# Kernel tuning notes

Measured on AMD Instinct MI355X. Metric: run time of the kernel, lower is better.

The kernel has to match this reference:

```python
import jax, jax.numpy as jnp
import numpy as np

B, L, D, H, DH, FF = 4, 1024, 1024, 16, 64, 4096
EPS = 1e-5


def _layer_norm(x, g, b):
    m = jnp.mean(x, -1, keepdims=True)
    v = jnp.mean((x - m) ** 2, -1, keepdims=True)
    return (x - m) * jax.lax.rsqrt(v + EPS) * g + b


def setup_inputs() -> dict:
    key = jax.random.key(0)
    ks = jax.random.split(key, 20)
    s = 0.02  # param init scale
    return {
        "x": jax.random.normal(ks[0], (B, L, D), jnp.float32),
        "adj_mask_matrix": jax.random.uniform(ks[1], (B * H, L, L), jnp.float32),
        "com_mask_matrix": jax.random.uniform(ks[2], (B * H, L, L), jnp.float32),
        "lattice_rel": jax.random.normal(ks[3], (2, 1, 1, DH), jnp.float32),
        "Wq": jax.random.normal(ks[4], (D, D), jnp.float32) * s,
        "bq": jnp.zeros((D,), jnp.float32),
        "Wk": jax.random.normal(ks[5], (D, D), jnp.float32) * s,
        "bk": jnp.zeros((D,), jnp.float32),
        "Wv": jax.random.normal(ks[6], (D, D), jnp.float32) * s,
        "bv": jnp.zeros((D,), jnp.float32),
        "Wo": jax.random.normal(ks[7], (D, D), jnp.float32) * s,
        "bo": jnp.zeros((D,), jnp.float32),
        "ln1_scale": jnp.ones((D,), jnp.float32),
        "ln1_bias": jnp.zeros((D,), jnp.float32),
        "W1": jax.random.normal(ks[8], (D, FF), jnp.float32) * s,
        "b1": jnp.zeros((FF,), jnp.float32),
        "W2": jax.random.normal(ks[9], (FF, D), jnp.float32) * s,
        "b2": jnp.zeros((D,), jnp.float32),
        "ln2_scale": jnp.ones((D,), jnp.float32),
        "ln2_bias": jnp.zeros((D,), jnp.float32),
    }


def reference(x, adj_mask_matrix, com_mask_matrix, lattice_rel,
              Wq, bq, Wk, bk, Wv, bv, Wo, bo, ln1_scale, ln1_bias,
              W1, b1, W2, b2, ln2_scale, ln2_bias):
    Bsz, Ln, Dm = x.shape
    # QKV projections; flat reshape [B,L,H*dh] -> [B*H,L,dh] matches torch .view
    Q = (x @ Wq + bq).reshape(Bsz * H, Ln, DH)
    K = (x @ Wk + bk).reshape(Bsz * H, Ln, DH)
    V = (x @ Wv + bv).reshape(Bsz * H, Ln, DH)
    scale = DH ** (-0.5)
    adj_rel = lattice_rel[0]  # [1,1,dh] broadcasts over (B*H, L)
    com_rel = lattice_rel[1]
    att_adj = jnp.einsum('bqd,bkd->bqk', Q + adj_rel, K + adj_rel) * scale
    att_com = jnp.einsum('bqd,bkd->bqk', Q + com_rel, K + com_rel) * scale
    # post-softmax multiplicative masking, then sum of the two attention maps
    mask_att = (jax.nn.softmax(att_adj, axis=-1) * adj_mask_matrix
                + jax.nn.softmax(att_com, axis=-1) * com_mask_matrix)
    context = jnp.matmul(mask_att, V).reshape(Bsz, Ln, H * DH)
    out = _layer_norm(context @ Wo + bo + x, ln1_scale, ln1_bias)
    ff = jax.nn.relu(out @ W1 + b1) @ W2 + b2
    return _layer_norm(ff + out, ln2_scale, ln2_bias)
```

## Files before the change

### kernel.cpp

```cpp
#include <hip/hip_runtime.h>
#include <hip/hip_bf16.h>

typedef __attribute__((ext_vector_type(8))) short s16x8;
typedef __attribute__((ext_vector_type(4))) float f32x4;
typedef unsigned short u16;
typedef unsigned int u32;

__device__ __forceinline__ u16 f2b(float f) {
    u32 u = __float_as_uint(f);
    u32 r = (u + 0x7fffu + ((u >> 16) & 1u)) >> 16;
    return (u16)r;
}
__device__ __forceinline__ float b2f(u16 b) {
    return __uint_as_float(((u32)b) << 16);
}

#define MFMA16(a, b, c) __builtin_amdgcn_mfma_f32_16x16x32_bf16(a, b, c, 0, 0, 0)
#define GLDS(gp, lp)                                                              \
    __builtin_amdgcn_global_load_lds((const __attribute__((address_space(1))) void*)(gp), \
                                     (__attribute__((address_space(3))) void*)(lp), 16, 0, 0)

__global__ void k_f2b(const float* __restrict__ in, u16* __restrict__ out, int n4) {
    int i = blockIdx.x * 256 + threadIdx.x;
    if (i >= n4) return;
    float4 v = ((const float4*)in)[i];
    ushort4 o;
    o.x = f2b(v.x); o.y = f2b(v.y); o.z = f2b(v.z); o.w = f2b(v.w);
    ((ushort4*)out)[i] = o;
}

__global__ void k_wtrans(const float* __restrict__ W, u16* __restrict__ Wt, int K, int N) {
    __shared__ float t[32][33];
    int bx = blockIdx.x * 32, by = blockIdx.y * 32;
    int tx = threadIdx.x, ty = threadIdx.y;
    for (int i = 0; i < 32; i += 8)
        t[ty + i][tx] = W[(size_t)(by + ty + i) * N + bx + tx];
    __syncthreads();
    for (int i = 0; i < 32; i += 8)
        Wt[(size_t)(bx + ty + i) * K + by + tx] = f2b(t[tx][ty + i]);
}

__global__ __launch_bounds__(256) void gemm_qkv(const u16* __restrict__ A, const u16* __restrict__ Bt,
                                                const float* __restrict__ bq, const float* __restrict__ bk,
                                                const float* __restrict__ bv, const float* __restrict__ rel,
                                                u16* __restrict__ Qa, u16* __restrict__ Qc,
                                                u16* __restrict__ Ka, u16* __restrict__ Kc,
                                                u16* __restrict__ Vt) {
    __shared__ __align__(16) short lA[128 * 64];
    __shared__ __align__(16) short lB[128 * 64];
    const int tid = threadIdx.x, lane = tid & 63, w = tid >> 6;
    const int l15 = lane & 15, lg = lane >> 4;
    const int wr = w >> 1, wc = w & 1;
    const int m0 = blockIdx.y * 128, n0 = blockIdx.x * 128;
    const int KK = 1024;
    f32x4 acc[4][4] = {};

    for (int k0 = 0; k0 < KK; k0 += 64) {
        #pragma unroll
        for (int i = 0; i < 4; i++) {
            int chunk = w * 4 + i;
            int arow = m0 + chunk * 8 + (lane >> 3);
            GLDS(A + (size_t)arow * KK + k0 + (lane & 7) * 8, (short*)lA + chunk * 512);
            int brow = n0 + chunk * 8 + (lane >> 3);
            GLDS(Bt + (size_t)brow * KK + k0 + (lane & 7) * 8, (short*)lB + chunk * 512);
        }
        __syncthreads();
        #pragma unroll
        for (int ks = 0; ks < 2; ks++) {
            s16x8 af[4], bfr[4];
            #pragma unroll
            for (int m = 0; m < 4; m++)
                af[m] = *(const s16x8*)&lA[(wr * 64 + m * 16 + l15) * 64 + ks * 32 + lg * 8];
            #pragma unroll
            for (int n = 0; n < 4; n++)
                bfr[n] = *(const s16x8*)&lB[(wc * 64 + n * 16 + l15) * 64 + ks * 32 + lg * 8];
            #pragma unroll
            for (int m = 0; m < 4; m++)
                #pragma unroll
                for (int n = 0; n < 4; n++)
                    acc[m][n] = MFMA16(af[m], bfr[n], acc[m][n]);
        }
        __syncthreads();
    }
    const int rbase = m0 + wr * 64, cbase = n0 + wc * 64;
    const int seg = cbase >> 10;
    #pragma unroll
    for (int m = 0; m < 4; m++)
        #pragma unroll
        for (int n = 0; n < 4; n++) {
            int col = cbase + n * 16 + l15;
            int c1 = col & 1023, d = col & 63;
            int row0 = rbase + m * 16 + lg * 4;
            if (seg == 0) {
                float bb = bq[c1], r0 = rel[d], r1 = rel[64 + d];
                #pragma unroll
                for (int r = 0; r < 4; r++) {
                    float v = acc[m][n][r] + bb;
                    size_t o = (size_t)(row0 + r) * 1024 + c1;
                    Qa[o] = f2b(v + r0);
                    Qc[o] = f2b(v + r1);
                }
            } else if (seg == 1) {
                float bb = bk[c1], r0 = rel[d], r1 = rel[64 + d];
                #pragma unroll
                for (int r = 0; r < 4; r++) {
                    float v = acc[m][n][r] + bb;
                    size_t o = (size_t)(row0 + r) * 1024 + c1;
                    Ka[o] = f2b(v + r0);
                    Kc[o] = f2b(v + r1);
                }
            } else {
                float bb = bv[c1];
                #pragma unroll
                for (int r = 0; r < 4; r++) {
                    int row = row0 + r;
                    size_t o = (size_t)(row >> 6) * 65536 + (size_t)d * 1024 + (row & 63) * 16 + (c1 >> 6);
                    Vt[o] = f2b(acc[m][n][r] + bb);
                }
            }
        }
}

template <int EPI>
__global__ __launch_bounds__(256) void gemm_bt(const u16* __restrict__ A, const u16* __restrict__ Bt,
                                               void* __restrict__ Cv, int M, int N, int K,
                                               const float* __restrict__ bias) {
    __shared__ __align__(16) short lA[128 * 64];
    __shared__ __align__(16) short lB[128 * 64];
    const int tid = threadIdx.x, lane = tid & 63, w = tid >> 6;
    const int l15 = lane & 15, lg = lane >> 4;
    const int wr = w >> 1, wc = w & 1;
    const int m0 = blockIdx.y * 128, n0 = blockIdx.x * 128;
    f32x4 acc[4][4] = {};

    for (int k0 = 0; k0 < K; k0 += 64) {
        #pragma unroll
        for (int i = 0; i < 4; i++) {
            int chunk = w * 4 + i;
            int arow = m0 + chunk * 8 + (lane >> 3);
            GLDS(A + (size_t)arow * K + k0 + (lane & 7) * 8, (short*)lA + chunk * 512);
            int brow = n0 + chunk * 8 + (lane >> 3);
            GLDS(Bt + (size_t)brow * K + k0 + (lane & 7) * 8, (short*)lB + chunk * 512);
        }
        __syncthreads();
        #pragma unroll
        for (int ks = 0; ks < 2; ks++) {
            s16x8 af[4], bfr[4];
            #pragma unroll
            for (int m = 0; m < 4; m++)
                af[m] = *(const s16x8*)&lA[(wr * 64 + m * 16 + l15) * 64 + ks * 32 + lg * 8];
            #pragma unroll
            for (int n = 0; n < 4; n++)
                bfr[n] = *(const s16x8*)&lB[(wc * 64 + n * 16 + l15) * 64 + ks * 32 + lg * 8];
            #pragma unroll
            for (int m = 0; m < 4; m++)
                #pragma unroll
                for (int n = 0; n < 4; n++)
                    acc[m][n] = MFMA16(af[m], bfr[n], acc[m][n]);
        }
        __syncthreads();
    }
    const int rbase = m0 + wr * 64, cbase = n0 + wc * 64;
    #pragma unroll
    for (int m = 0; m < 4; m++)
        #pragma unroll
        for (int n = 0; n < 4; n++) {
            int col = cbase + n * 16 + l15;
            int row0 = rbase + m * 16 + lg * 4;
            u16* C = (u16*)Cv;
            float bv = bias[col];
            #pragma unroll
            for (int r = 0; r < 4; r++)
                C[(size_t)(row0 + r) * N + col] = f2b(fmaxf(acc[m][n][r] + bv, 0.f));
        }
}

__global__ __launch_bounds__(256) void gemm_bt64(const u16* __restrict__ A, const u16* __restrict__ Bt,
                                                 float* __restrict__ C, int M, int N, int K) {
    __shared__ __align__(16) short lA[128 * 64];
    __shared__ __align__(16) short lB[64 * 64];
    const int tid = threadIdx.x, lane = tid & 63, w = tid >> 6;
    const int l15 = lane & 15, lg = lane >> 4;
    const int m0 = blockIdx.y * 128, n0 = blockIdx.x * 64;
    f32x4 acc[2][4] = {};

    for (int k0 = 0; k0 < K; k0 += 64) {
        #pragma unroll
        for (int i = 0; i < 4; i++) {
            int chunk = w * 4 + i;
            int arow = m0 + chunk * 8 + (lane >> 3);
            GLDS(A + (size_t)arow * K + k0 + (lane & 7) * 8, (short*)lA + chunk * 512);
        }
        #pragma unroll
        for (int i = 0; i < 2; i++) {
            int chunk = w * 2 + i;
            int brow = n0 + chunk * 8 + (lane >> 3);
            GLDS(Bt + (size_t)brow * K + k0 + (lane & 7) * 8, (short*)lB + chunk * 512);
        }
        __syncthreads();
        #pragma unroll
        for (int ks = 0; ks < 2; ks++) {
            s16x8 af[2], bfr[4];
            #pragma unroll
            for (int m = 0; m < 2; m++)
                af[m] = *(const s16x8*)&lA[(w * 32 + m * 16 + l15) * 64 + ks * 32 + lg * 8];
            #pragma unroll
            for (int n = 0; n < 4; n++)
                bfr[n] = *(const s16x8*)&lB[(n * 16 + l15) * 64 + ks * 32 + lg * 8];
            #pragma unroll
            for (int m = 0; m < 2; m++)
                #pragma unroll
                for (int n = 0; n < 4; n++)
                    acc[m][n] = MFMA16(af[m], bfr[n], acc[m][n]);
        }
        __syncthreads();
    }
    #pragma unroll
    for (int m = 0; m < 2; m++)
        #pragma unroll
        for (int n = 0; n < 4; n++) {
            int col = n0 + n * 16 + l15;
            int row0 = m0 + w * 32 + m * 16 + lg * 4;
            #pragma unroll
            for (int r = 0; r < 4; r++)
                C[(size_t)(row0 + r) * N + col] = acc[m][n][r];
        }
}

__global__ __launch_bounds__(256, 2) void k_qke2(const u16* __restrict__ Qa, const u16* __restrict__ Qc,
                                                 const u16* __restrict__ Ka, const u16* __restrict__ Kc,
                                                 u16* __restrict__ Ea, u16* __restrict__ Ec,
                                                 float* __restrict__ denA, float* __restrict__ denC) {
    const int bid = blockIdx.x;
    const int xcd = bid & 7, j = bid >> 3;
    const int g = xcd * 8 + (j & 7), qt = j >> 3;
    const int tid = threadIdx.x, lane = tid & 63, w = tid >> 6;
    const int l15 = lane & 15, lg = lane >> 4;
    __shared__ __align__(16) float lE[2][4][16][68];

    const int q0 = qt * 64 + w * 16;
    const size_t gQ = (size_t)g * 65536;
    const size_t ebase = ((((size_t)g * 16 + qt) * 4 + w) * 16384) + (size_t)lane * 8;
    const float scale = 0.125f;

    s16x8 qa[2], qc[2];
    #pragma unroll
    for (int ks = 0; ks < 2; ks++) {
        size_t off = gQ + (size_t)(q0 + l15) * 64 + ks * 32 + lg * 8;
        qa[ks] = *(const s16x8*)(Qa + off);
        qc[ks] = *(const s16x8*)(Qc + off);
    }

    float la[4] = {0.f, 0.f, 0.f, 0.f}, lc[4] = {0.f, 0.f, 0.f, 0.f};

    #pragma unroll 1
    for (int it = 0; it < 16; it++) {
        const int kb = it * 64;
        f32x4 sa[4] = {}, sc[4] = {};
        s16x8 kfa[8], kfc[8];
        #pragma unroll
        for (int ks = 0; ks < 2; ks++)
            #pragma unroll
            for (int n = 0; n < 4; n++) {
                size_t koff = gQ + (size_t)(kb + n * 16 + l15) * 64 + ks * 32 + lg * 8;
                kfa[ks * 4 + n] = *(const s16x8*)(Ka + koff);
                kfc[ks * 4 + n] = *(const s16x8*)(Kc + koff);
            }
        #pragma unroll
        for (int ks = 0; ks < 2; ks++)
            #pragma unroll
            for (int n = 0; n < 4; n++) {
                sa[n] = MFMA16(qa[ks], kfa[ks * 4 + n], sa[n]);
                sc[n] = MFMA16(qc[ks], kfc[ks * 4 + n], sc[n]);
            }
        #pragma unroll
        for (int n = 0; n < 4; n++)
            #pragma unroll
            for (int r = 0; r < 4; r++) {
                float ea = __expf(sa[n][r] * scale);
                float ec = __expf(sc[n][r] * scale);
                la[r] += ea;
                lc[r] += ec;
                lE[0][w][lg * 4 + r][n * 16 + l15] = ea;
                lE[1][w][lg * 4 + r][n * 16 + l15] = ec;
            }
        #pragma unroll
        for (int ks = 0; ks < 2; ks++) {
            const float* ep = &lE[0][w][l15][ks * 32 + lg * 8];
            float4 e0 = *(const float4*)ep, e1 = *(const float4*)(ep + 4);
            uint4 st;
            st.x = (u32)f2b(e0.x) | ((u32)f2b(e0.y) << 16);
            st.y = (u32)f2b(e0.z) | ((u32)f2b(e0.w) << 16);
            st.z = (u32)f2b(e1.x) | ((u32)f2b(e1.y) << 16);
            st.w = (u32)f2b(e1.z) | ((u32)f2b(e1.w) << 16);
            *(uint4*)(Ea + ebase + (size_t)it * 1024 + ks * 512) = st;
            const float* fp = &lE[1][w][l15][ks * 32 + lg * 8];
            float4 f0 = *(const float4*)fp, f1 = *(const float4*)(fp + 4);
            uint4 st2;
            st2.x = (u32)f2b(f0.x) | ((u32)f2b(f0.y) << 16);
            st2.y = (u32)f2b(f0.z) | ((u32)f2b(f0.w) << 16);
            st2.z = (u32)f2b(f1.x) | ((u32)f2b(f1.y) << 16);
            st2.w = (u32)f2b(f1.z) | ((u32)f2b(f1.w) << 16);
            *(uint4*)(Ec + ebase + (size_t)it * 1024 + ks * 512) = st2;
        }
    }
    #pragma unroll
    for (int r = 0; r < 4; r++)
        #pragma unroll
        for (int m = 8; m >= 1; m >>= 1) {
            la[r] += __shfl_xor(la[r], m);
            lc[r] += __shfl_xor(lc[r], m);
        }
    if (l15 == 0) {
        #pragma unroll
        for (int r = 0; r < 4; r++) {
            denA[g * 1024 + q0 + lg * 4 + r] = la[r];
            denC[g * 1024 + q0 + lg * 4 + r] = lc[r];
        }
    }
}

__global__ __launch_bounds__(256, 2) void k_pv2(const u16* __restrict__ Ea, const u16* __restrict__ Ec,
                                                const u16* __restrict__ Vt,
                                                const float* __restrict__ adjm, const float* __restrict__ comm,
                                                const float* __restrict__ denA, const float* __restrict__ denC,
                                                u16* __restrict__ ctx) {
    const int bid = blockIdx.x;
    const int xcd = bid & 7, j = bid >> 3;
    const int g = xcd * 8 + (j & 7), qt = j >> 3;
    const int tid = threadIdx.x, lane = tid & 63, w = tid >> 6;
    const int l15 = lane & 15, lg = lane >> 4;

    const int q0 = qt * 64 + w * 16;
    const size_t gQ = (size_t)g * 65536;
    const size_t mroff = (size_t)g * 1048576 + (size_t)(q0 + l15) * 1024 + lg * 8;
    const float* __restrict__ mrow_a = adjm + mroff;
    const float* __restrict__ mrow_c = comm + mroff;
    const size_t ebase = ((((size_t)g * 16 + qt) * 4 + w) * 16384) + (size_t)lane * 8;

    f32x4 ca[4] = {}, cc[4] = {};

    #pragma unroll 2
    for (int it = 0; it < 16; it++) {
        const int kb = it * 64;
        s16x8 ea[2], ec[2], vf[8];
        float4 ma[4], mc[4];
        #pragma unroll
        for (int ks = 0; ks < 2; ks++) {
            ma[ks * 2 + 0] = *(const float4*)(mrow_a + kb + ks * 32);
            ma[ks * 2 + 1] = *(const float4*)(mrow_a + kb + ks * 32 + 4);
            mc[ks * 2 + 0] = *(const float4*)(mrow_c + kb + ks * 32);
            mc[ks * 2 + 1] = *(const float4*)(mrow_c + kb + ks * 32 + 4);
        }
        #pragma unroll
        for (int ks = 0; ks < 2; ks++) {
            ea[ks] = *(const s16x8*)(Ea + ebase + (size_t)it * 1024 + ks * 512);
            ec[ks] = *(const s16x8*)(Ec + ebase + (size_t)it * 1024 + ks * 512);
        }
        #pragma unroll
        for (int ks = 0; ks < 2; ks++)
            #pragma unroll
            for (int d = 0; d < 4; d++)
                vf[ks * 4 + d] = *(const s16x8*)(Vt + gQ + (size_t)(d * 16 + l15) * 1024 + kb + ks * 32 + lg * 8);
        #pragma unroll
        for (int ks = 0; ks < 2; ks++) {
            union { s16x8 v; u16 u[8]; } pa, pc;
            pa.u[0] = f2b(b2f((u16)ea[ks][0]) * ma[ks * 2].x);
            pa.u[1] = f2b(b2f((u16)ea[ks][1]) * ma[ks * 2].y);
            pa.u[2] = f2b(b2f((u16)ea[ks][2]) * ma[ks * 2].z);
            pa.u[3] = f2b(b2f((u16)ea[ks][3]) * ma[ks * 2].w);
            pa.u[4] = f2b(b2f((u16)ea[ks][4]) * ma[ks * 2 + 1].x);
            pa.u[5] = f2b(b2f((u16)ea[ks][5]) * ma[ks * 2 + 1].y);
            pa.u[6] = f2b(b2f((u16)ea[ks][6]) * ma[ks * 2 + 1].z);
            pa.u[7] = f2b(b2f((u16)ea[ks][7]) * ma[ks * 2 + 1].w);
            pc.u[0] = f2b(b2f((u16)ec[ks][0]) * mc[ks * 2].x);
            pc.u[1] = f2b(b2f((u16)ec[ks][1]) * mc[ks * 2].y);
            pc.u[2] = f2b(b2f((u16)ec[ks][2]) * mc[ks * 2].z);
            pc.u[3] = f2b(b2f((u16)ec[ks][3]) * mc[ks * 2].w);
            pc.u[4] = f2b(b2f((u16)ec[ks][4]) * mc[ks * 2 + 1].x);
            pc.u[5] = f2b(b2f((u16)ec[ks][5]) * mc[ks * 2 + 1].y);
            pc.u[6] = f2b(b2f((u16)ec[ks][6]) * mc[ks * 2 + 1].z);
            pc.u[7] = f2b(b2f((u16)ec[ks][7]) * mc[ks * 2 + 1].w);
            #pragma unroll
            for (int d = 0; d < 4; d++) {
                ca[d] = MFMA16(pa.v, vf[ks * 4 + d], ca[d]);
                cc[d] = MFMA16(pc.v, vf[ks * 4 + d], cc[d]);
            }
        }
    }
    float ila[4], ilc[4];
    #pragma unroll
    for (int r = 0; r < 4; r++) {
        ila[r] = 1.f / denA[g * 1024 + q0 + lg * 4 + r];
        ilc[r] = 1.f / denC[g * 1024 + q0 + lg * 4 + r];
    }
    #pragma unroll
    for (int r = 0; r < 4; r++) {
        int row = q0 + lg * 4 + r;
        #pragma unroll
        for (int d = 0; d < 4; d++)
            ctx[gQ + (size_t)row * 64 + d * 16 + l15] = f2b(ca[d][r] * ila[r] + cc[d][r] * ilc[r]);
    }
}

__global__ __launch_bounds__(256) void k_ln(const float* __restrict__ a, const float* __restrict__ bias,
                                            const float* __restrict__ resid, const float* __restrict__ gamma,
                                            const float* __restrict__ beta, float* __restrict__ out,
                                            u16* __restrict__ outb) {
    const int row = blockIdx.x, tid = threadIdx.x;
    const size_t base = (size_t)row * 1024 + tid * 4;
    float4 av = *(const float4*)(a + base);
    float4 rv = *(const float4*)(resid + base);
    float4 bv = *(const float4*)(bias + tid * 4);
    float t0 = av.x + rv.x + bv.x, t1 = av.y + rv.y + bv.y;
    float t2 = av.z + rv.z + bv.z, t3 = av.w + rv.w + bv.w;
    __shared__ float red[4];
    float s = t0 + t1 + t2 + t3;
    #pragma unroll
    for (int m = 32; m >= 1; m >>= 1) s += __shfl_xor(s, m);
    int w = tid >> 6;
    if ((tid & 63) == 0) red[w] = s;
    __syncthreads();
    float mean = (red[0] + red[1] + red[2] + red[3]) * (1.f / 1024.f);
    float d0 = t0 - mean, d1 = t1 - mean, d2 = t2 - mean, d3 = t3 - mean;
    float q = d0 * d0 + d1 * d1 + d2 * d2 + d3 * d3;
    __syncthreads();
    #pragma unroll
    for (int m = 32; m >= 1; m >>= 1) q += __shfl_xor(q, m);
    if ((tid & 63) == 0) red[w] = q;
    __syncthreads();
    float var = (red[0] + red[1] + red[2] + red[3]) * (1.f / 1024.f);
    float rs = rsqrtf(var + 1e-5f);
    float4 gv = *(const float4*)(gamma + tid * 4);
    float4 bev = *(const float4*)(beta + tid * 4);
    float o0 = d0 * rs * gv.x + bev.x, o1 = d1 * rs * gv.y + bev.y;
    float o2 = d2 * rs * gv.z + bev.z, o3 = d3 * rs * gv.w + bev.w;
    *(float4*)(out + base) = make_float4(o0, o1, o2, o3);
    if (outb) {
        ushort4 ob;
        ob.x = f2b(o0); ob.y = f2b(o1); ob.z = f2b(o2); ob.w = f2b(o3);
        *(ushort4*)(outb + base) = ob;
    }
}

extern "C" void kernel_launch(void* const* d_in, const int* in_sizes, int n_in,
                              void* d_out, int out_size, void* d_ws, size_t ws_size,
                              hipStream_t stream) {
    const float* x    = (const float*)d_in[0];
    const float* adjm = (const float*)d_in[1];
    const float* comm = (const float*)d_in[2];
    const float* rel  = (const float*)d_in[3];
    const float* Wq   = (const float*)d_in[4];
    const float* bq   = (const float*)d_in[5];
    const float* Wk   = (const float*)d_in[6];
    const float* bk   = (const float*)d_in[7];
    const float* Wv   = (const float*)d_in[8];
    const float* bv   = (const float*)d_in[9];
    const float* Wo   = (const float*)d_in[10];
    const float* bo   = (const float*)d_in[11];
    const float* g1   = (const float*)d_in[12];
    const float* be1  = (const float*)d_in[13];
    const float* W1   = (const float*)d_in[14];
    const float* b1   = (const float*)d_in[15];
    const float* W2   = (const float*)d_in[16];
    const float* b2   = (const float*)d_in[17];
    const float* g2   = (const float*)d_in[18];
    const float* be2  = (const float*)d_in[19];
    float* out = (float*)d_out;

    char* ws = (char*)d_ws;
    const size_t MB = 1048576;
    u16*   xb    = (u16*)(ws + 0 * MB);
    u16*   Wqkvt = (u16*)(ws + 8 * MB);
    u16*   Wot   = (u16*)(ws + 14 * MB);
    u16*   W1t   = (u16*)(ws + 16 * MB);
    u16*   W2t   = (u16*)(ws + 24 * MB);
    u16*   Qab   = (u16*)(ws + 32 * MB);
    u16*   Qcb   = (u16*)(ws + 40 * MB);
    u16*   Kab   = (u16*)(ws + 48 * MB);
    u16*   Kcb   = (u16*)(ws + 56 * MB);
    u16*   Vtb   = (u16*)(ws + 64 * MB);
    u16*   Eab   = (u16*)(ws + 72 * MB);
    u16*   Ecb   = (u16*)(ws + 200 * MB);
    float* denA  = (float*)(ws + 328 * MB);
    float* denC  = (float*)(ws + 329 * MB);
    u16*   ctx   = (u16*)(ws + 330 * MB);
    float* ctxWo = (float*)(ws + 32 * MB);
    float* out1  = (float*)(ws + 48 * MB);
    u16*   out1b = (u16*)(ws + 64 * MB);
    u16*   rb    = (u16*)(ws + 72 * MB);
    float* ff2   = (float*)(ws + 0 * MB);

    dim3 tb(32, 8);
    k_f2b<<<4096, 256, 0, stream>>>(x, xb, 1048576);
    k_wtrans<<<dim3(32, 32), tb, 0, stream>>>(Wq, Wqkvt, 1024, 1024);
    k_wtrans<<<dim3(32, 32), tb, 0, stream>>>(Wk, Wqkvt + 1024 * 1024, 1024, 1024);
    k_wtrans<<<dim3(32, 32), tb, 0, stream>>>(Wv, Wqkvt + 2 * 1024 * 1024, 1024, 1024);
    k_wtrans<<<dim3(32, 32), tb, 0, stream>>>(Wo, Wot, 1024, 1024);
    k_wtrans<<<dim3(128, 32), tb, 0, stream>>>(W1, W1t, 1024, 4096);
    k_wtrans<<<dim3(32, 128), tb, 0, stream>>>(W2, W2t, 4096, 1024);
    gemm_qkv<<<dim3(24, 32), 256, 0, stream>>>(xb, Wqkvt, bq, bk, bv, rel,
                                               Qab, Qcb, Kab, Kcb, Vtb);
    k_qke2<<<1024, 256, 0, stream>>>(Qab, Qcb, Kab, Kcb, Eab, Ecb, denA, denC);
    k_pv2<<<1024, 256, 0, stream>>>(Eab, Ecb, Vtb, adjm, comm, denA, denC, ctx);
    gemm_bt64<<<dim3(16, 32), 256, 0, stream>>>(ctx, Wot, ctxWo, 4096, 1024, 1024);
    k_ln<<<4096, 256, 0, stream>>>(ctxWo, bo, x, g1, be1, out1, out1b);
    gemm_bt<1><<<dim3(32, 32), 256, 0, stream>>>(out1b, W1t, rb, 4096, 4096, 1024, b1);
    gemm_bt64<<<dim3(16, 32), 256, 0, stream>>>(rb, W2t, ff2, 4096, 1024, 4096);
    k_ln<<<4096, 256, 0, stream>>>(ff2, b2, out1, g2, be2, out, nullptr);
}
```

Baseline: 654.1 us.

## Split attention key dimension in two halves with partial sums and combine kernel

The QK-exp and PV attention kernels now split the 1024 keys into two halves, doubling the grid from 1024 to 2048 blocks. Each half writes its own partial softmax denominators and an fp32 partial context. PV sums the two denominator halves before normalizing, and a new combine kernel adds the two partial contexts and converts them to bf16. This buys more parallelism per launch, but costs an extra fp32 write and read of the context, one more launch, and more denominator traffic.

```diff
diff --git a/kernel.cpp b/kernel.cpp
--- a/kernel.cpp
+++ b/kernel.cpp
@@ -230,10 +230,12 @@
 __global__ __launch_bounds__(256, 2) void k_qke2(const u16* __restrict__ Qa, const u16* __restrict__ Qc,
                                                  const u16* __restrict__ Ka, const u16* __restrict__ Kc,
                                                  u16* __restrict__ Ea, u16* __restrict__ Ec,
-                                                 float* __restrict__ denA, float* __restrict__ denC) {
+                                                 float* __restrict__ denA2, float* __restrict__ denC2) {
     const int bid = blockIdx.x;
     const int xcd = bid & 7, j = bid >> 3;
-    const int g = xcd * 8 + (j & 7), qt = j >> 3;
+    const int g = xcd * 8 + (j & 7);
+    const int rest = j >> 3;
+    const int qt = rest & 15, h = rest >> 4;
     const int tid = threadIdx.x, lane = tid & 63, w = tid >> 6;
     const int l15 = lane & 15, lg = lane >> 4;
     __shared__ __align__(16) float lE[2][4][16][68];
@@ -254,7 +256,7 @@
     float la[4] = {0.f, 0.f, 0.f, 0.f}, lc[4] = {0.f, 0.f, 0.f, 0.f};
 
     #pragma unroll 1
-    for (int it = 0; it < 16; it++) {
+    for (int it = h * 8; it < h * 8 + 8; it++) {
         const int kb = it * 64;
         f32x4 sa[4] = {}, sc[4] = {};
         s16x8 kfa[8], kfc[8];
@@ -314,8 +316,8 @@
     if (l15 == 0) {
         #pragma unroll
         for (int r = 0; r < 4; r++) {
-            denA[g * 1024 + q0 + lg * 4 + r] = la[r];
-            denC[g * 1024 + q0 + lg * 4 + r] = lc[r];
+            denA2[h * 65536 + g * 1024 + q0 + lg * 4 + r] = la[r];
+            denC2[h * 65536 + g * 1024 + q0 + lg * 4 + r] = lc[r];
         }
     }
 }
@@ -323,11 +325,13 @@
 __global__ __launch_bounds__(256, 2) void k_pv2(const u16* __restrict__ Ea, const u16* __restrict__ Ec,
                                                 const u16* __restrict__ Vt,
                                                 const float* __restrict__ adjm, const float* __restrict__ comm,
-                                                const float* __restrict__ denA, const float* __restrict__ denC,
-                                                u16* __restrict__ ctx) {
+                                                const float* __restrict__ denA2, const float* __restrict__ denC2,
+                                                float* __restrict__ ctxP) {
     const int bid = blockIdx.x;
     const int xcd = bid & 7, j = bid >> 3;
-    const int g = xcd * 8 + (j & 7), qt = j >> 3;
+    const int g = xcd * 8 + (j & 7);
+    const int rest = j >> 3;
+    const int qt = rest & 15, h = rest >> 4;
     const int tid = threadIdx.x, lane = tid & 63, w = tid >> 6;
     const int l15 = lane & 15, lg = lane >> 4;
 
@@ -341,7 +345,7 @@
     f32x4 ca[4] = {}, cc[4] = {};
 
     #pragma unroll 2
-    for (int it = 0; it < 16; it++) {
+    for (int it = h * 8; it < h * 8 + 8; it++) {
         const int kb = it * 64;
         s16x8 ea[2], ec[2], vf[8];
         float4 ma[4], mc[4];
@@ -391,16 +395,29 @@
     float ila[4], ilc[4];
     #pragma unroll
     for (int r = 0; r < 4; r++) {
-        ila[r] = 1.f / denA[g * 1024 + q0 + lg * 4 + r];
-        ilc[r] = 1.f / denC[g * 1024 + q0 + lg * 4 + r];
+        int idx = g * 1024 + q0 + lg * 4 + r;
+        ila[r] = 1.f / (denA2[idx] + denA2[65536 + idx]);
+        ilc[r] = 1.f / (denC2[idx] + denC2[65536 + idx]);
     }
     #pragma unroll
     for (int r = 0; r < 4; r++) {
         int row = q0 + lg * 4 + r;
         #pragma unroll
         for (int d = 0; d < 4; d++)
-            ctx[gQ + (size_t)row * 64 + d * 16 + l15] = f2b(ca[d][r] * ila[r] + cc[d][r] * ilc[r]);
-    }
+            ctxP[(size_t)h * 4194304 + gQ + (size_t)row * 64 + d * 16 + l15] =
+                ca[d][r] * ila[r] + cc[d][r] * ilc[r];
+    }
+}
+
+__global__ void k_comb2(const float* __restrict__ P, u16* __restrict__ out, int n4) {
+    int i = blockIdx.x * 256 + threadIdx.x;
+    if (i >= n4) return;
+    float4 a = ((const float4*)P)[i];
+    float4 c = ((const float4*)(P + 4194304))[i];
+    ushort4 o;
+    o.x = f2b(a.x + c.x); o.y = f2b(a.y + c.y);
+    o.z = f2b(a.z + c.z); o.w = f2b(a.w + c.w);
+    ((ushort4*)out)[i] = o;
 }
 
 __global__ __launch_bounds__(256) void k_ln(const float* __restrict__ a, const float* __restrict__ bias,
@@ -482,9 +499,10 @@
     u16*   Vtb   = (u16*)(ws + 64 * MB);
     u16*   Eab   = (u16*)(ws + 72 * MB);
     u16*   Ecb   = (u16*)(ws + 200 * MB);
-    float* denA  = (float*)(ws + 328 * MB);
-    float* denC  = (float*)(ws + 329 * MB);
-    u16*   ctx   = (u16*)(ws + 330 * MB);
+    float* denA2 = (float*)(ws + 328 * MB);
+    float* denC2 = (float*)(ws + 329 * MB);
+    float* ctxP  = (float*)(ws + 330 * MB);
+    u16*   ctx   = (u16*)(ws + 362 * MB);
     float* ctxWo = (float*)(ws + 32 * MB);
     float* out1  = (float*)(ws + 48 * MB);
     u16*   out1b = (u16*)(ws + 64 * MB);
@@ -501,8 +519,9 @@
     k_wtrans<<<dim3(32, 128), tb, 0, stream>>>(W2, W2t, 4096, 1024);
     gemm_qkv<<<dim3(24, 32), 256, 0, stream>>>(xb, Wqkvt, bq, bk, bv, rel,
                                                Qab, Qcb, Kab, Kcb, Vtb);
-    k_qke2<<<1024, 256, 0, stream>>>(Qab, Qcb, Kab, Kcb, Eab, Ecb, denA, denC);
-    k_pv2<<<1024, 256, 0, stream>>>(Eab, Ecb, Vtb, adjm, comm, denA, denC, ctx);
+    k_qke2<<<2048, 256, 0, stream>>>(Qab, Qcb, Kab, Kcb, Eab, Ecb, denA2, denC2);
+    k_pv2<<<2048, 256, 0, stream>>>(Eab, Ecb, Vtb, adjm, comm, denA2, denC2, ctxP);
+    k_comb2<<<4096, 256, 0, stream>>>(ctxP, ctx, 1048576);
     gemm_bt64<<<dim3(16, 32), 256, 0, stream>>>(ctx, Wot, ctxWo, 4096, 1024, 1024);
     k_ln<<<4096, 256, 0, stream>>>(ctxWo, bo, x, g1, be1, out1, out1b);
     gemm_bt<1><<<dim3(32, 32), 256, 0, stream>>>(out1b, W1t, rb, 4096, 4096, 1024, b1);
```

Result: no change. 646.6 us (-1.1%).
